# Kernel tuning notes

Hardware: AMD Instinct MI355X
Metric: run time of the kernel (lower is better)

The kernel has to match this reference:

```python
import jax, jax.numpy as jnp
import numpy as np

N = 50000          # nodes
E = 800000         # edges (avg degree 16)
F = 128            # in_dim = num_hidden*heads = pred_dim
H = 4              # attention heads per layer
D = 32             # num_hidden (per-head dim)
R = 11             # rel_num
L = 2              # num_layers
SCALE = float(1.0 / np.sqrt(D))


def setup_inputs() -> dict:
    key = jax.random.key(0)
    ks = jax.random.split(key, 16)
    inputs = jax.random.normal(ks[0], (N, F), jnp.float32)
    edge_types = jax.random.randint(ks[1], (E,), 0, R)
    src = jax.random.randint(ks[2], (E,), 0, N)
    dst = jax.random.randint(ks[3], (E,), 0, N)
    centrality = jax.random.uniform(ks[4], (N,), jnp.float32)
    rel_emb = jax.random.normal(ks[5], (R, F), jnp.float32) * 0.1
    # stacked per-layer projection weights (both layers have F -> H*D = F)
    Wq = jax.random.normal(ks[6], (L, F, H * D), jnp.float32) * 0.05
    Wk = jax.random.normal(ks[7], (L, F, H * D), jnp.float32) * 0.05
    Wv = jax.random.normal(ks[8], (L, F, H * D), jnp.float32) * 0.05
    We = jax.random.normal(ks[9], (L, F, H * D), jnp.float32) * 0.05
    bq = jnp.zeros((L, H * D), jnp.float32)
    bk = jnp.zeros((L, H * D), jnp.float32)
    bv = jnp.zeros((L, H * D), jnp.float32)
    be = jnp.zeros((L, H * D), jnp.float32)
    W_out = jax.random.normal(ks[10], (H * D, 1), jnp.float32) * 0.05
    b_out = jnp.zeros((1,), jnp.float32)
    gamma = jnp.ones((1,), jnp.float32)
    beta = jnp.zeros((1,), jnp.float32)
    return {"inputs": inputs, "edge_types": edge_types, "src": src, "dst": dst,
            "centrality": centrality, "rel_emb": rel_emb,
            "Wq": Wq, "bq": bq, "Wk": Wk, "bk": bk, "Wv": Wv, "bv": bv,
            "We": We, "be": be, "W_out": W_out, "b_out": b_out,
            "gamma": gamma, "beta": beta}


def _segment_softmax(score, dst, n):
    # score: [E, H]; softmax over incoming edges of each dst node
    m = jax.ops.segment_max(score, dst, num_segments=n)          # [N, H]
    ex = jnp.exp(score - m[dst])                                  # [E, H]
    s = jax.ops.segment_sum(ex, dst, num_segments=n)              # [N, H]
    return ex / (s[dst] + 1e-9)


def reference(inputs, edge_types, src, dst, centrality, rel_emb,
              Wq, bq, Wk, bk, Wv, bv, We, be, W_out, b_out, gamma, beta):
    h = inputs                                   # [N, F]
    ef = rel_emb[edge_types]                     # [E, pred_dim] relational edge embedding
    for l in range(L):
        q = (h @ Wq[l] + bq[l]).reshape(N, H, D)
        k = (h @ Wk[l] + bk[l]).reshape(N, H, D)
        v = (h @ Wv[l] + bv[l]).reshape(N, H, D)
        e = (ef @ We[l] + be[l]).reshape(E, H, D)
        # edge_mode="add": edge features added to keys/values on each edge
        ke = k[src] + e                           # [E, H, D]
        score = jnp.sum(q[dst] * ke, axis=-1) * SCALE   # [E, H]
        attn = _segment_softmax(score, dst, N)          # [E, H]
        msg = attn[:, :, None] * (v[src] + e)           # [E, H, D]
        agg = jax.ops.segment_sum(msg, dst, num_segments=N)  # [N, H, D]
        # identity residual (in_dim == H*D) + ELU activation
        h = jax.nn.elu(agg.reshape(N, H * D) + h)
    logits = h @ W_out + b_out                    # [N, 1]
    logits = jax.nn.relu((centrality * gamma + beta)[:, None] * logits)
    return logits
```

## Files before the change

kernel.cpp:

```cpp
#include <hip/hip_runtime.h>
#include <hip/hip_bf16.h>
#include <math.h>

#define SCALE_C 0.17677669529663687f

typedef short bf16x8 __attribute__((ext_vector_type(8)));
typedef float f32x4 __attribute__((ext_vector_type(4)));


__global__ __launch_bounds__(256) void count_k(const int* __restrict__ dst, int E, int* __restrict__ counts) {
  int e = blockIdx.x * 256 + threadIdx.x;
  if (e < E) atomicAdd(&counts[dst[e]], 1);
}

__global__ __launch_bounds__(256) void scanA_k(const int* __restrict__ counts, int* __restrict__ offs,
                                               int* __restrict__ partial, int n) {
  __shared__ int sd[256];
  int t = threadIdx.x;
  int i = blockIdx.x * 256 + t;
  int v = (i < n) ? counts[i] : 0;
  sd[t] = v;
  __syncthreads();
  for (int off = 1; off < 256; off <<= 1) {
    int x = (t >= off) ? sd[t - off] : 0;
    __syncthreads();
    sd[t] += x;
    __syncthreads();
  }
  if (i < n) offs[i] = sd[t] - v;
  if (t == 255) partial[blockIdx.x] = sd[255];
}

__global__ __launch_bounds__(256) void scanB_k(const int* __restrict__ partial, int* __restrict__ partial2,
                                               int nb, int* __restrict__ offs, int n, int total) {
  __shared__ int sd[256];
  int t = threadIdx.x;
  int v = (t < nb) ? partial[t] : 0;
  sd[t] = v;
  __syncthreads();
  for (int off = 1; off < 256; off <<= 1) {
    int x = (t >= off) ? sd[t - off] : 0;
    __syncthreads();
    sd[t] += x;
    __syncthreads();
  }
  if (t < nb) partial2[t] = sd[t] - v;
  if (t == 0) offs[n] = total;
}

__global__ __launch_bounds__(256) void scanC_k(int* __restrict__ offs, const int* __restrict__ partial2, int n) {
  int i = blockIdx.x * 256 + threadIdx.x;
  if (i < n) offs[i] += partial2[blockIdx.x];
}

__global__ __launch_bounds__(256) void scatter_k(const int* __restrict__ dst, const int* __restrict__ src,
                                                 const int* __restrict__ etype, int E,
                                                 const int* __restrict__ offs, int* __restrict__ cursor,
                                                 int* __restrict__ packed) {
  int e = blockIdx.x * 256 + threadIdx.x;
  if (e < E) {
    int d = dst[e];
    int pos = atomicAdd(&cursor[d], 1);
    packed[offs[d] + pos] = src[e] | (etype[e] << 20);
  }
}


__global__ __launch_bounds__(256) void prep_k(
    const float* __restrict__ Wq, const float* __restrict__ Wk, const float* __restrict__ Wv,
    __hip_bfloat16* __restrict__ wf,
    const float* __restrict__ rel_emb, const float* __restrict__ We, const float* __restrict__ be,
    float* __restrict__ re, int R) {
  int b = blockIdx.x;
  if (b < 48) {
    int tid = b * 256 + threadIdx.x;
    int lane = tid & 63;
    int frag = tid >> 6;
    int ks = frag & 3;
    int ct = (frag >> 2) & 7;
    int mat = frag >> 5;
    int l = mat / 3, m = mat % 3;
    const float* W = ((m == 0) ? Wq : (m == 1) ? Wk : Wv) + (size_t)l * 128 * 128;
    int nn = ct * 16 + (lane & 15);
    int k0 = ks * 32 + (lane >> 4) * 8;
    __hip_bfloat16 tmp[8];
    #pragma unroll
    for (int j = 0; j < 8; ++j) tmp[j] = __float2bfloat16(W[(size_t)(k0 + j) * 128 + nn]);
    *(uint4*)&wf[(size_t)frag * 64 * 8 + (size_t)lane * 8] = *(const uint4*)tmp;
  } else {
    int idx = (b - 48) * 256 + threadIdx.x;
    int tot = 2 * R * 128;
    if (idx >= tot) return;
    int c = idx & 127;
    int r = (idx >> 7) % R;
    int l = idx / (R * 128);
    const float* W = We + (size_t)l * 128 * 128;
    float acc = be[l * 128 + c];
    for (int kk = 0; kk < 128; ++kk) acc += rel_emb[r * 128 + kk] * W[kk * 128 + c];
    re[idx] = acc;
  }
}


__global__ __launch_bounds__(128) void qkv_k(
    const float* __restrict__ X, const __hip_bfloat16* __restrict__ wf,
    const float* __restrict__ bq, const float* __restrict__ bk, const float* __restrict__ bv,
    float* __restrict__ qo, __hip_bfloat16* __restrict__ kvo, int n) {
  __shared__ __hip_bfloat16 kvt[2][32][264];
  int wid = threadIdx.x >> 6;
  int lane = threadIdx.x & 63;
  int row0 = blockIdx.x * 64 + wid * 32;
  if (row0 >= n) return;
  int cl = lane & 15;
  int quad = lane >> 4;

  bf16x8 afrag[2][4];
  #pragma unroll
  for (int s = 0; s < 2; ++s) {
    int arow = row0 + s * 16 + cl;
    bool av = arow < n;
    const float* xr = X + (size_t)arow * 128 + quad * 8;
    #pragma unroll
    for (int ks = 0; ks < 4; ++ks) {
      float4 x0 = av ? *(const float4*)(xr + ks * 32)     : make_float4(0.f, 0.f, 0.f, 0.f);
      float4 x1 = av ? *(const float4*)(xr + ks * 32 + 4) : make_float4(0.f, 0.f, 0.f, 0.f);
      union { bf16x8 v; __hip_bfloat16 h[8]; } fu;
      fu.h[0] = __float2bfloat16(x0.x); fu.h[1] = __float2bfloat16(x0.y);
      fu.h[2] = __float2bfloat16(x0.z); fu.h[3] = __float2bfloat16(x0.w);
      fu.h[4] = __float2bfloat16(x1.x); fu.h[5] = __float2bfloat16(x1.y);
      fu.h[6] = __float2bfloat16(x1.z); fu.h[7] = __float2bfloat16(x1.w);
      afrag[s][ks] = fu.v;
    }
  }
  const uint4* wfu = (const uint4*)wf;

  #pragma unroll
  for (int ct = 0; ct < 8; ++ct) {
    f32x4 a0 = {0.f, 0.f, 0.f, 0.f}, a1 = {0.f, 0.f, 0.f, 0.f};
    #pragma unroll
    for (int ks = 0; ks < 4; ++ks) {
      uint4 braw = wfu[((size_t)ct * 4 + ks) * 64 + lane];
      bf16x8 bfr = __builtin_bit_cast(bf16x8, braw);
      a0 = __builtin_amdgcn_mfma_f32_16x16x32_bf16(afrag[0][ks], bfr, a0, 0, 0, 0);
      a1 = __builtin_amdgcn_mfma_f32_16x16x32_bf16(afrag[1][ks], bfr, a1, 0, 0, 0);
    }
    int c = ct * 16 + cl;
    float bb = bq[c];
    #pragma unroll
    for (int r = 0; r < 4; ++r) {
      int row = row0 + quad * 4 + r;
      if (row < n) qo[(size_t)row * 128 + c] = a0[r] + bb;
      if (row + 16 < n) qo[(size_t)(row + 16) * 128 + c] = a1[r] + bb;
    }
  }

  #pragma unroll
  for (int m = 1; m <= 2; ++m) {
    const float* bias = (m == 1) ? bk : bv;
    #pragma unroll
    for (int ct = 0; ct < 8; ++ct) {
      f32x4 a0 = {0.f, 0.f, 0.f, 0.f}, a1 = {0.f, 0.f, 0.f, 0.f};
      #pragma unroll
      for (int ks = 0; ks < 4; ++ks) {
        uint4 braw = wfu[((size_t)(m * 8 + ct) * 4 + ks) * 64 + lane];
        bf16x8 bfr = __builtin_bit_cast(bf16x8, braw);
        a0 = __builtin_amdgcn_mfma_f32_16x16x32_bf16(afrag[0][ks], bfr, a0, 0, 0, 0);
        a1 = __builtin_amdgcn_mfma_f32_16x16x32_bf16(afrag[1][ks], bfr, a1, 0, 0, 0);
      }
      int c = ct * 16 + cl;
      float bb = bias[c];
      int p = 8 * (c >> 2) + (c & 3) + ((m == 2) ? 4 : 0);
      #pragma unroll
      for (int r = 0; r < 4; ++r) {
        kvt[wid][quad * 4 + r][p]      = __float2bfloat16(a0[r] + bb);
        kvt[wid][16 + quad * 4 + r][p] = __float2bfloat16(a1[r] + bb);
      }
    }
  }

  const uint4* tsrc = (const uint4*)&kvt[wid][0][0];
  #pragma unroll
  for (int it = 0; it < 16; ++it) {
    int idx = it * 64 + lane;
    int row = idx >> 5, off = idx & 31;
    if (row0 + row < n)
      *(uint4*)&kvo[((size_t)(row0 + row)) * 256 + off * 8] = tsrc[row * 33 + off];
  }
}


__global__ __launch_bounds__(256) void edge_k(
    const float* __restrict__ q, const __hip_bfloat16* __restrict__ kv,
    const float* __restrict__ re,
    const int* __restrict__ packed, const int* __restrict__ offs,
    const float* __restrict__ h_in, float* __restrict__ h_out,
    const float* __restrict__ Wout, const float* __restrict__ bout,
    const float* __restrict__ cent, const float* __restrict__ gamma,
    const float* __restrict__ beta, float* __restrict__ outp, int n) {
  int node = blockIdx.x * 4 + (threadIdx.x >> 6);
  if (node >= n) return;
  int lane = threadIdx.x & 63;
  int j = lane & 15;
  int quarter = lane >> 4;
  int rs = offs[node];
  int deg = offs[node + 1] - rs;

  const float4* qrow = (const float4*)q + ((uint)node * 32u + (uint)(j * 2));
  float4 qa = qrow[0], qb = qrow[1];
  qa.x *= SCALE_C; qa.y *= SCALE_C; qa.z *= SCALE_C; qa.w *= SCALE_C;
  qb.x *= SCALE_C; qb.y *= SCALE_C; qb.z *= SCALE_C; qb.w *= SCALE_C;

  float ssum = 0.f;
  float acc0 = 0.f, acc1 = 0.f, acc2 = 0.f, acc3 = 0.f;
  float acc4 = 0.f, acc5 = 0.f, acc6 = 0.f, acc7 = 0.f;
  int nit = (deg + 3) >> 2;
  int pk = (quarter < deg) ? packed[rs + quarter] : 0;
  for (int i = 0; i < nit; ++i) {
    int eidx = 4 * i + quarter;
    bool valid = eidx < deg;
    uint s_ = (uint)pk & 0xFFFFFu;
    uint t_ = (uint)pk >> 20;
    int en = eidx + 4;
    int pk_n = (en < deg) ? packed[rs + en] : 0;
    const uint4* kr = (const uint4*)kv + (s_ * 32u + (uint)(j * 2));
    uint4 raw0 = kr[0];
    uint4 raw1 = kr[1];
    const float4* rr = (const float4*)re + (t_ * 32u + (uint)(j * 2));
    float4 r0 = rr[0];
    float4 r1 = rr[1];
    float k0 = __uint_as_float(raw0.x << 16);
    float k1 = __uint_as_float(raw0.x & 0xffff0000u);
    float k2 = __uint_as_float(raw0.y << 16);
    float k3 = __uint_as_float(raw0.y & 0xffff0000u);
    float v0 = __uint_as_float(raw0.z << 16);
    float v1 = __uint_as_float(raw0.z & 0xffff0000u);
    float v2 = __uint_as_float(raw0.w << 16);
    float v3 = __uint_as_float(raw0.w & 0xffff0000u);
    float k4 = __uint_as_float(raw1.x << 16);
    float k5 = __uint_as_float(raw1.x & 0xffff0000u);
    float k6 = __uint_as_float(raw1.y << 16);
    float k7 = __uint_as_float(raw1.y & 0xffff0000u);
    float v4 = __uint_as_float(raw1.z << 16);
    float v5 = __uint_as_float(raw1.z & 0xffff0000u);
    float v6 = __uint_as_float(raw1.w << 16);
    float v7 = __uint_as_float(raw1.w & 0xffff0000u);
    float p = qa.x * (k0 + r0.x) + qa.y * (k1 + r0.y) + qa.z * (k2 + r0.z) + qa.w * (k3 + r0.w)
            + qb.x * (k4 + r1.x) + qb.y * (k5 + r1.y) + qb.z * (k6 + r1.z) + qb.w * (k7 + r1.w);
    p += __shfl_xor(p, 1);
    p += __shfl_xor(p, 2);
    float w = valid ? __expf(p) : 0.f;
    ssum += w;
    acc0 += w * (v0 + r0.x);
    acc1 += w * (v1 + r0.y);
    acc2 += w * (v2 + r0.z);
    acc3 += w * (v3 + r0.w);
    acc4 += w * (v4 + r1.x);
    acc5 += w * (v5 + r1.y);
    acc6 += w * (v6 + r1.z);
    acc7 += w * (v7 + r1.w);
    pk = pk_n;
  }
  ssum += __shfl_xor(ssum, 16); ssum += __shfl_xor(ssum, 32);
  acc0 += __shfl_xor(acc0, 16); acc0 += __shfl_xor(acc0, 32);
  acc1 += __shfl_xor(acc1, 16); acc1 += __shfl_xor(acc1, 32);
  acc2 += __shfl_xor(acc2, 16); acc2 += __shfl_xor(acc2, 32);
  acc3 += __shfl_xor(acc3, 16); acc3 += __shfl_xor(acc3, 32);
  acc4 += __shfl_xor(acc4, 16); acc4 += __shfl_xor(acc4, 32);
  acc5 += __shfl_xor(acc5, 16); acc5 += __shfl_xor(acc5, 32);
  acc6 += __shfl_xor(acc6, 16); acc6 += __shfl_xor(acc6, 32);
  acc7 += __shfl_xor(acc7, 16); acc7 += __shfl_xor(acc7, 32);
  if (quarter != 0) return;

  float inv = 1.f / (ssum + 1e-9f);
  const float4* hrow = (const float4*)h_in + ((uint)node * 32u + (uint)(j * 2));
  float4 h0 = hrow[0], h1 = hrow[1];
  float x0 = acc0 * inv + h0.x;
  float x1 = acc1 * inv + h0.y;
  float x2 = acc2 * inv + h0.z;
  float x3 = acc3 * inv + h0.w;
  float x4 = acc4 * inv + h1.x;
  float x5 = acc5 * inv + h1.y;
  float x6 = acc6 * inv + h1.z;
  float x7 = acc7 * inv + h1.w;
  x0 = x0 > 0.f ? x0 : expm1f(x0);
  x1 = x1 > 0.f ? x1 : expm1f(x1);
  x2 = x2 > 0.f ? x2 : expm1f(x2);
  x3 = x3 > 0.f ? x3 : expm1f(x3);
  x4 = x4 > 0.f ? x4 : expm1f(x4);
  x5 = x5 > 0.f ? x5 : expm1f(x5);
  x6 = x6 > 0.f ? x6 : expm1f(x6);
  x7 = x7 > 0.f ? x7 : expm1f(x7);
  if (outp == nullptr) {
    float4* orow = (float4*)h_out + ((uint)node * 32u + (uint)(j * 2));
    orow[0] = make_float4(x0, x1, x2, x3);
    orow[1] = make_float4(x4, x5, x6, x7);
  } else {
    const float4* wrow = (const float4*)Wout + (uint)(j * 2);
    float4 w0 = wrow[0], w1 = wrow[1];
    float pp = x0 * w0.x + x1 * w0.y + x2 * w0.z + x3 * w0.w
             + x4 * w1.x + x5 * w1.y + x6 * w1.z + x7 * w1.w;
    pp += __shfl_xor(pp, 1);
    pp += __shfl_xor(pp, 2);
    pp += __shfl_xor(pp, 4);
    pp += __shfl_xor(pp, 8);
    if (lane == 0) {
      float lg = pp + bout[0];
      lg *= (cent[node] * gamma[0] + beta[0]);
      outp[node] = fmaxf(lg, 0.f);
    }
  }
}


extern "C" void kernel_launch(void* const* d_in, const int* in_sizes, int n_in,
                              void* d_out, int out_size, void* d_ws, size_t ws_size,
                              hipStream_t stream) {
  const float* inputs  = (const float*)d_in[0];
  const int*   etype   = (const int*)d_in[1];
  const int*   src     = (const int*)d_in[2];
  const int*   dst     = (const int*)d_in[3];
  const float* cent    = (const float*)d_in[4];
  const float* rel_emb = (const float*)d_in[5];
  const float* Wq      = (const float*)d_in[6];
  const float* bq      = (const float*)d_in[7];
  const float* Wk      = (const float*)d_in[8];
  const float* bk      = (const float*)d_in[9];
  const float* Wv      = (const float*)d_in[10];
  const float* bv      = (const float*)d_in[11];
  const float* We      = (const float*)d_in[12];
  const float* be      = (const float*)d_in[13];
  const float* Wout    = (const float*)d_in[14];
  const float* bout    = (const float*)d_in[15];
  const float* gamma   = (const float*)d_in[16];
  const float* beta    = (const float*)d_in[17];
  float* out = (float*)d_out;

  const int N = in_sizes[0] / 128;
  const int E = in_sizes[1];
  const int R = in_sizes[5] / 128;

  float* fw   = (float*)d_ws;
  float* q    = fw;
  float* hbuf = q + (size_t)N * 128;
  float* re   = hbuf + (size_t)N * 128;
  __hip_bfloat16* kv = (__hip_bfloat16*)(re + 2 * (size_t)R * 128);
  __hip_bfloat16* wf = kv + (size_t)N * 256;
  int* counts   = (int*)(wf + 6 * 16384);
  int* cursor   = counts + N;
  int* offs     = cursor + N;
  int* partial  = offs + N + 1;
  int* partial2 = partial + 256;
  int* packed   = partial2 + 256;

  hipMemsetAsync(counts, 0, 2 * (size_t)N * sizeof(int), stream);

  int ebl = (E + 255) / 256;
  int nb = (N + 255) / 256;
  count_k<<<ebl, 256, 0, stream>>>(dst, E, counts);
  scanA_k<<<nb, 256, 0, stream>>>(counts, offs, partial, N);
  scanB_k<<<1, 256, 0, stream>>>(partial, partial2, nb, offs, N, E);
  scanC_k<<<nb, 256, 0, stream>>>(offs, partial2, N);
  scatter_k<<<ebl, 256, 0, stream>>>(dst, src, etype, E, offs, cursor, packed);
  prep_k<<<48 + (2 * R * 128 + 255) / 256, 256, 0, stream>>>(Wq, Wk, Wv, wf, rel_emb, We, be, re, R);

  int qb = (N + 63) / 64;
  int eb = (N + 3) / 4;
  for (int l = 0; l < 2; ++l) {
    const float* X = (l == 0) ? inputs : hbuf;
    size_t bo = (size_t)l * 128;
    qkv_k<<<qb, 128, 0, stream>>>(X, wf + (size_t)l * 3 * 16384,
                                  bq + bo, bk + bo, bv + bo, q, kv, N);
    edge_k<<<eb, 256, 0, stream>>>(q, kv, re + (size_t)l * R * 128, packed, offs, X, hbuf,
                                   Wout, bout, cent, gamma, beta,
                                   (l == 1) ? out : nullptr, N);
  }
}
```

Before: 361.5 us.

## Fold scan fixup into consumers and merge scanB with weight prep kernel

The separate scanC offset-fixup kernel is removed; scatter_k and edge_k now add the block prefix partial2[node>>8] when reading offs. The top-level scan is merged into the prep kernel as block 0, cutting two kernel launches from the CSR build. The final offset entry is stored pre-biased so the same formula works for node N. qkv_k also shrinks its shared staging buffer to a per-matrix K/V tile and writes interleaved 8-byte chunks after each matrix instead of one 16-byte pass, trading wider stores for less LDS.

After: 372.4 us. +3.0%, slower.

```diff
diff --git a/kernel.cpp b/kernel.cpp
--- a/kernel.cpp
+++ b/kernel.cpp
@@ -31,49 +31,30 @@
   if (t == 255) partial[blockIdx.x] = sd[255];
 }
 
-__global__ __launch_bounds__(256) void scanB_k(const int* __restrict__ partial, int* __restrict__ partial2,
-                                               int nb, int* __restrict__ offs, int n, int total) {
-  __shared__ int sd[256];
-  int t = threadIdx.x;
-  int v = (t < nb) ? partial[t] : 0;
-  sd[t] = v;
-  __syncthreads();
-  for (int off = 1; off < 256; off <<= 1) {
-    int x = (t >= off) ? sd[t - off] : 0;
-    __syncthreads();
-    sd[t] += x;
-    __syncthreads();
-  }
-  if (t < nb) partial2[t] = sd[t] - v;
-  if (t == 0) offs[n] = total;
-}
-
-__global__ __launch_bounds__(256) void scanC_k(int* __restrict__ offs, const int* __restrict__ partial2, int n) {
-  int i = blockIdx.x * 256 + threadIdx.x;
-  if (i < n) offs[i] += partial2[blockIdx.x];
-}
-
-__global__ __launch_bounds__(256) void scatter_k(const int* __restrict__ dst, const int* __restrict__ src,
-                                                 const int* __restrict__ etype, int E,
-                                                 const int* __restrict__ offs, int* __restrict__ cursor,
-                                                 int* __restrict__ packed) {
-  int e = blockIdx.x * 256 + threadIdx.x;
-  if (e < E) {
-    int d = dst[e];
-    int pos = atomicAdd(&cursor[d], 1);
-    packed[offs[d] + pos] = src[e] | (etype[e] << 20);
-  }
-}
-
-
-__global__ __launch_bounds__(256) void prep_k(
+__global__ __launch_bounds__(256) void scanB_prep_k(
+    const int* __restrict__ partial, int* __restrict__ partial2, int nb,
+    int* __restrict__ offs, int n, int total,
     const float* __restrict__ Wq, const float* __restrict__ Wk, const float* __restrict__ Wv,
     __hip_bfloat16* __restrict__ wf,
     const float* __restrict__ rel_emb, const float* __restrict__ We, const float* __restrict__ be,
     float* __restrict__ re, int R) {
   int b = blockIdx.x;
-  if (b < 48) {
-    int tid = b * 256 + threadIdx.x;
+  if (b == 0) {
+    __shared__ int sd[256];
+    int t = threadIdx.x;
+    int v = (t < nb) ? partial[t] : 0;
+    sd[t] = v;
+    __syncthreads();
+    for (int off = 1; off < 256; off <<= 1) {
+      int x = (t >= off) ? sd[t - off] : 0;
+      __syncthreads();
+      sd[t] += x;
+      __syncthreads();
+    }
+    if (t < nb) partial2[t] = sd[t] - v;
+    if (t == nb - 1) offs[n] = total - (sd[t] - v);
+  } else if (b <= 48) {
+    int tid = (b - 1) * 256 + threadIdx.x;
     int lane = tid & 63;
     int frag = tid >> 6;
     int ks = frag & 3;
@@ -88,7 +69,7 @@
     for (int j = 0; j < 8; ++j) tmp[j] = __float2bfloat16(W[(size_t)(k0 + j) * 128 + nn]);
     *(uint4*)&wf[(size_t)frag * 64 * 8 + (size_t)lane * 8] = *(const uint4*)tmp;
   } else {
-    int idx = (b - 48) * 256 + threadIdx.x;
+    int idx = (b - 49) * 256 + threadIdx.x;
     int tot = 2 * R * 128;
     if (idx >= tot) return;
     int c = idx & 127;
@@ -101,12 +82,24 @@
   }
 }
 
+__global__ __launch_bounds__(256) void scatter_k(const int* __restrict__ dst, const int* __restrict__ src,
+                                                 const int* __restrict__ etype, int E,
+                                                 const int* __restrict__ offs, const int* __restrict__ partial2,
+                                                 int* __restrict__ cursor, int* __restrict__ packed) {
+  int e = blockIdx.x * 256 + threadIdx.x;
+  if (e < E) {
+    int d = dst[e];
+    int pos = atomicAdd(&cursor[d], 1);
+    packed[offs[d] + partial2[d >> 8] + pos] = src[e] | (etype[e] << 20);
+  }
+}
+
 
 __global__ __launch_bounds__(128) void qkv_k(
     const float* __restrict__ X, const __hip_bfloat16* __restrict__ wf,
     const float* __restrict__ bq, const float* __restrict__ bk, const float* __restrict__ bv,
     float* __restrict__ qo, __hip_bfloat16* __restrict__ kvo, int n) {
-  __shared__ __hip_bfloat16 kvt[2][32][264];
+  __shared__ __hip_bfloat16 kt[2][32][136];
   int wid = threadIdx.x >> 6;
   int lane = threadIdx.x & 63;
   int row0 = blockIdx.x * 64 + wid * 32;
@@ -169,22 +162,21 @@
       }
       int c = ct * 16 + cl;
       float bb = bias[c];
-      int p = 8 * (c >> 2) + (c & 3) + ((m == 2) ? 4 : 0);
       #pragma unroll
       for (int r = 0; r < 4; ++r) {
-        kvt[wid][quad * 4 + r][p]      = __float2bfloat16(a0[r] + bb);
-        kvt[wid][16 + quad * 4 + r][p] = __float2bfloat16(a1[r] + bb);
+        kt[wid][quad * 4 + r][c]      = __float2bfloat16(a0[r] + bb);
+        kt[wid][16 + quad * 4 + r][c] = __float2bfloat16(a1[r] + bb);
       }
     }
-  }
-
-  const uint4* tsrc = (const uint4*)&kvt[wid][0][0];
-  #pragma unroll
-  for (int it = 0; it < 16; ++it) {
-    int idx = it * 64 + lane;
-    int row = idx >> 5, off = idx & 31;
-    if (row0 + row < n)
-      *(uint4*)&kvo[((size_t)(row0 + row)) * 256 + off * 8] = tsrc[row * 33 + off];
+    int voff = (m == 2) ? 1 : 0;
+    #pragma unroll
+    for (int it = 0; it < 16; ++it) {
+      int idx = it * 64 + lane;
+      int row = idx >> 5, g = idx & 31;
+      if (row0 + row < n)
+        ((uint2*)(kvo + ((size_t)(row0 + row)) * 256))[2 * g + voff] =
+            *(const uint2*)&kt[wid][row][4 * g];
+    }
   }
 }
 
@@ -193,6 +185,7 @@
     const float* __restrict__ q, const __hip_bfloat16* __restrict__ kv,
     const float* __restrict__ re,
     const int* __restrict__ packed, const int* __restrict__ offs,
+    const int* __restrict__ partial2,
     const float* __restrict__ h_in, float* __restrict__ h_out,
     const float* __restrict__ Wout, const float* __restrict__ bout,
     const float* __restrict__ cent, const float* __restrict__ gamma,
@@ -202,8 +195,9 @@
   int lane = threadIdx.x & 63;
   int j = lane & 15;
   int quarter = lane >> 4;
-  int rs = offs[node];
-  int deg = offs[node + 1] - rs;
+  int rs = offs[node] + partial2[node >> 8];
+  int rend = offs[node + 1] + partial2[(node + 1) >> 8];
+  int deg = rend - rs;
 
   const float4* qrow = (const float4*)q + ((uint)node * 32u + (uint)(j * 2));
   float4 qa = qrow[0], qb = qrow[1];
@@ -358,10 +352,10 @@
   int nb = (N + 255) / 256;
   count_k<<<ebl, 256, 0, stream>>>(dst, E, counts);
   scanA_k<<<nb, 256, 0, stream>>>(counts, offs, partial, N);
-  scanB_k<<<1, 256, 0, stream>>>(partial, partial2, nb, offs, N, E);
-  scanC_k<<<nb, 256, 0, stream>>>(offs, partial2, N);
-  scatter_k<<<ebl, 256, 0, stream>>>(dst, src, etype, E, offs, cursor, packed);
-  prep_k<<<48 + (2 * R * 128 + 255) / 256, 256, 0, stream>>>(Wq, Wk, Wv, wf, rel_emb, We, be, re, R);
+  int prep_blocks = 1 + 48 + (2 * R * 128 + 255) / 256;
+  scanB_prep_k<<<prep_blocks, 256, 0, stream>>>(partial, partial2, nb, offs, N, E,
+                                                Wq, Wk, Wv, wf, rel_emb, We, be, re, R);
+  scatter_k<<<ebl, 256, 0, stream>>>(dst, src, etype, E, offs, partial2, cursor, packed);
 
   int qb = (N + 63) / 64;
   int eb = (N + 3) / 4;
@@ -370,8 +364,8 @@
     size_t bo = (size_t)l * 128;
     qkv_k<<<qb, 128, 0, stream>>>(X, wf + (size_t)l * 3 * 16384,
                                   bq + bo, bk + bo, bv + bo, q, kv, N);
-    edge_k<<<eb, 256, 0, stream>>>(q, kv, re + (size_t)l * R * 128, packed, offs, X, hbuf,
-                                   Wout, bout, cent, gamma, beta,
+    edge_k<<<eb, 256, 0, stream>>>(q, kv, re + (size_t)l * R * 128, packed, offs, partial2,
+                                   X, hbuf, Wout, bout, cent, gamma, beta,
                                    (l == 1) ? out : nullptr, N);
   }
 }
```
